# Optimization experiments

Hardware: AMD Instinct MI355X
Metric: run time of the kernel (lower is better)

## Reference

```python
import jax, jax.numpy as jnp
import numpy as np

NQ = 10          # num_qubits
NL = 4           # num_layers (StronglyEntanglingLayers)
DIM = 2 ** NQ    # state-vector dimension = input_linear out features
B = 4096
SEQ = 512
PRED = 96

# ---- static basis-state bookkeeping (wire 0 = most significant bit, as in PennyLane) ----

def _cnot_perm(control, target):
    s = np.arange(DIM)
    bit = (s >> (NQ - 1 - control)) & 1
    return s ^ (bit << (NQ - 1 - target))

def _layer_perms():
    # StronglyEntanglingLayers default ranges: r_l = (l % (n_wires - 1)) + 1,
    # then CNOT(i, (i+r) % n) for i = 0..n-1, applied sequentially.
    perms = []
    for l in range(NL):
        r = (l % (NQ - 1)) + 1
        comp = np.arange(DIM)
        for c in range(NQ):
            g = _cnot_perm(c, (c + r) % NQ)
            comp = comp[g]          # compose: state_new[t] = state_old[comp[t]]
        perms.append(jnp.asarray(comp))
    return perms

PERMS = _layer_perms()

_bits = (np.arange(DIM)[:, None] >> (NQ - 1 - np.arange(NQ))[None, :]) & 1
SIGNS = jnp.asarray(1.0 - 2.0 * _bits, dtype=np.float32)   # [DIM, NQ] PauliZ eigenvalues


def _rot_gates(w):
    # PennyLane Rot(phi, theta, omega) = RZ(omega) @ RY(theta) @ RZ(phi); w: [L, n, 3]
    phi, theta, omega = w[..., 0], w[..., 1], w[..., 2]
    c = jnp.cos(theta / 2)
    s = jnp.sin(theta / 2)
    ep = jnp.exp(0.5j * (phi + omega))   # e^{+i(phi+omega)/2}
    em = jnp.exp(0.5j * (phi - omega))   # e^{+i(phi-omega)/2}
    m00 = jnp.conj(ep) * c
    m01 = -em * s
    m10 = jnp.conj(em) * s
    m11 = ep * c
    return jnp.stack([jnp.stack([m00, m01], -1),
                      jnp.stack([m10, m11], -1)], -2)       # [L, n, 2, 2] complex64


def _apply_1q(psi, U, wire):
    # psi: [B, DIM] complex; apply 2x2 U on `wire`
    b = psi.shape[0]
    left = 2 ** wire
    right = 2 ** (NQ - 1 - wire)
    psi = psi.reshape(b, left, 2, right)
    psi = jnp.einsum('ba,kpaq->kpbq', U, psi)
    return psi.reshape(b, DIM)


def _circuit(psi, q_weights):
    mats = _rot_gates(q_weights)
    for l in range(NL):
        for w in range(NQ):
            psi = _apply_1q(psi, mats[l, w], w)
        psi = psi[:, PERMS[l]]          # composed CNOT ring of this layer
    return psi


def reference(x, W_in, b_in, q_weights, W_out, b_out):
    h = x @ W_in.T + b_in + 1e-6                          # input_linear, then +1e-6
    norm = jnp.linalg.norm(h, axis=-1, keepdims=True)
    psi = (h / norm).astype(jnp.complex64)                # AmplitudeEmbedding(normalize=True)
    psi = _circuit(psi, q_weights)                        # StronglyEntanglingLayers
    probs = psi.real ** 2 + psi.imag ** 2
    expvals = probs @ SIGNS                               # [B, NQ] PauliZ expvals
    return expvals @ W_out.T + b_out                      # output_linear


def setup_inputs() -> dict:
    key = jax.random.key(0)
    ks = jax.random.split(key, 6)
    x = jax.random.normal(ks[0], (B, SEQ), dtype=jnp.float32)
    W_in = jax.random.normal(ks[1], (DIM, SEQ), dtype=jnp.float32) / np.sqrt(SEQ)
    b_in = jax.random.normal(ks[2], (DIM,), dtype=jnp.float32) * 0.01
    q_weights = jax.random.uniform(ks[3], (NL, NQ, 3), dtype=jnp.float32,
                                   minval=0.0, maxval=2.0 * np.pi)
    W_out = jax.random.normal(ks[4], (PRED, NQ), dtype=jnp.float32) / np.sqrt(NQ)
    b_out = jax.random.normal(ks[5], (PRED,), dtype=jnp.float32) * 0.01
    return {"x": x, "W_in": W_in, "b_in": b_in, "q_weights": q_weights,
            "W_out": W_out, "b_out": b_out}
```

## Files before the change

### kernel.cpp

```cpp
#include <hip/hip_runtime.h>
#include <math.h>

#define DIM 1024
#define NQ 10
#define NL 4
#define SEQ 512
#define NROWS 4096
#define PRED 96

typedef unsigned short ushort_t;
typedef unsigned int uint_t;
using half8   = __attribute__((ext_vector_type(8))) _Float16;
using float4v = __attribute__((ext_vector_type(4))) float;

__device__ inline ushort_t f2h(float f) { _Float16 h = (_Float16)f; return *(ushort_t*)&h; }
__device__ inline uint_t pkh(float a, float b) {
    _Float16 ha = (_Float16)a, hb = (_Float16)b;
    return (uint_t)(*(ushort_t*)&ha) | ((uint_t)(*(ushort_t*)&hb) << 16);
}

#define CVT_BLOCKS 1024
#define TRN_BLOCKS 128

__global__ __launch_bounds__(256)
void convert_x_kernel(const float* __restrict__ x, ushort_t* __restrict__ xh,
                      const float* __restrict__ Wi, float* __restrict__ WiT)
{
    __shared__ float t[64][65];
    const int tid = threadIdx.x;
    const int bid = blockIdx.x;

    if (bid < CVT_BLOCKS) {
        int i = (bid * 256 + tid) * 8;
        float4 a = *(const float4*)(x + i);
        float4 b = *(const float4*)(x + i + 4);
        uint4 o;
        o.x = pkh(a.x, a.y); o.y = pkh(a.z, a.w);
        o.z = pkh(b.x, b.y); o.w = pkh(b.z, b.w);
        *(uint4*)(xh + i) = o;
    } else {
        const int b = bid - CVT_BLOCKS;
        const int s0 = (b & 15) * 64;
        const int j0 = (b >> 4) * 64;
        {
            const int r = tid >> 2, cs = (tid & 3) * 16;
            const float* src = Wi + (size_t)(s0 + r) * SEQ + j0 + cs;
            float4 v0 = *(const float4*)(src);
            float4 v1 = *(const float4*)(src + 4);
            float4 v2 = *(const float4*)(src + 8);
            float4 v3 = *(const float4*)(src + 12);
            t[r][cs + 0] = v0.x; t[r][cs + 1] = v0.y; t[r][cs + 2] = v0.z; t[r][cs + 3] = v0.w;
            t[r][cs + 4] = v1.x; t[r][cs + 5] = v1.y; t[r][cs + 6] = v1.z; t[r][cs + 7] = v1.w;
            t[r][cs + 8] = v2.x; t[r][cs + 9] = v2.y; t[r][cs +10] = v2.z; t[r][cs +11] = v2.w;
            t[r][cs +12] = v3.x; t[r][cs +13] = v3.y; t[r][cs +14] = v3.z; t[r][cs +15] = v3.w;
        }
        __syncthreads();
        {
            const int jj = tid >> 2, ss = (tid & 3) * 16;
            float* dst = WiT + (size_t)(j0 + jj) * DIM + s0 + ss;
#pragma unroll
            for (int seg = 0; seg < 4; ++seg) {
                float4 o;
                o.x = t[ss + seg * 4 + 0][jj];
                o.y = t[ss + seg * 4 + 1][jj];
                o.z = t[ss + seg * 4 + 2][jj];
                o.w = t[ss + seg * 4 + 3][jj];
                *(float4*)(dst + seg * 4) = o;
            }
        }
    }
}

__global__ __launch_bounds__(256)
void circuit_hybrid_kernel(const float* __restrict__ WiT, const float* __restrict__ b_in,
                           const float* __restrict__ qw,
                           ushort_t* __restrict__ Crt_r, ushort_t* __restrict__ Crt_i,
                           float* __restrict__ dr, float* __restrict__ di)
{
    __shared__ float gm[NL * NQ][8];
    __shared__ float bre[2][DIM];
    __shared__ float bim[2][DIM];

    const int tid = threadIdx.x;
    const int j = blockIdx.x;

    if (tid < NL * NQ) {
        float phi = qw[tid * 3 + 0], theta = qw[tid * 3 + 1], omega = qw[tid * 3 + 2];
        float ch = cosf(theta * 0.5f), sh = sinf(theta * 0.5f);
        float a = 0.5f * (phi + omega), b = 0.5f * (phi - omega);
        float ca = cosf(a), sa = sinf(a);
        float cb = cosf(b), sb = sinf(b);
        gm[tid][0] =  ch * ca;  gm[tid][1] = -ch * sa;
        gm[tid][2] = -sh * cb;  gm[tid][3] = -sh * sb;
        gm[tid][4] =  sh * cb;  gm[tid][5] = -sh * sb;
        gm[tid][6] =  ch * ca;  gm[tid][7] =  ch * sa;
    }

    float2 st[4];
    if (j < SEQ) {
        float4 wv = *(const float4*)(WiT + (size_t)j * DIM + tid * 4);
        st[0] = make_float2(wv.x, 0.f);
        st[1] = make_float2(wv.y, 0.f);
        st[2] = make_float2(wv.z, 0.f);
        st[3] = make_float2(wv.w, 0.f);
    } else {
#pragma unroll
        for (int r = 0; r < 4; ++r)
            st[r] = make_float2(b_in[tid * 4 + r] + 1e-6f, 0.f);
    }
#pragma unroll
    for (int r = 0; r < 4; ++r) {
        bre[0][r * 256 + tid] = st[r].x;
        bim[0][r * 256 + tid] = st[r].y;
    }
    __syncthreads();
    int cur = 0;

    {
        const float* m = gm[0];
        const int hi = tid >> 7;
        float cAr = hi ? m[6] : m[0], cAi = hi ? m[7] : m[1];
        float cBr = hi ? m[4] : m[2], cBi = hi ? m[5] : m[3];
#pragma unroll
        for (int r = 0; r < 4; ++r) {
            float px = bre[cur][r * 256 + (tid ^ 128)];
            float py = bim[cur][r * 256 + (tid ^ 128)];
            float nx = cAr * st[r].x - cAi * st[r].y + cBr * px - cBi * py;
            float ny = cAr * st[r].y + cAi * st[r].x + cBr * py + cBi * px;
            st[r] = make_float2(nx, ny);
        }
    }

#pragma unroll
    for (int l = 0; l < NL; ++l) {
        {
#pragma unroll
            for (int r = 0; r < 4; ++r) {
                bre[cur ^ 1][r * 256 + tid] = st[r].x;
                bim[cur ^ 1][r * 256 + tid] = st[r].y;
            }
            __syncthreads();
            cur ^= 1;
            const float* m = gm[l * NQ + 1];
            const int hi = (tid >> 6) & 1;
            float cAr = hi ? m[6] : m[0], cAi = hi ? m[7] : m[1];
            float cBr = hi ? m[4] : m[2], cBi = hi ? m[5] : m[3];
#pragma unroll
            for (int r = 0; r < 4; ++r) {
                float px = bre[cur][r * 256 + (tid ^ 64)];
                float py = bim[cur][r * 256 + (tid ^ 64)];
                float nx = cAr * st[r].x - cAi * st[r].y + cBr * px - cBi * py;
                float ny = cAr * st[r].y + cAi * st[r].x + cBr * py + cBi * px;
                st[r] = make_float2(nx, ny);
            }
        }
#pragma unroll
        for (int w = 2; w < 8; ++w) {
            const float* m = gm[l * NQ + w];
            const int lb = 7 - w;
            const int hi = (tid >> lb) & 1;
            float cAr = hi ? m[6] : m[0], cAi = hi ? m[7] : m[1];
            float cBr = hi ? m[4] : m[2], cBi = hi ? m[5] : m[3];
            const int mask = 1 << lb;
#pragma unroll
            for (int r = 0; r < 4; ++r) {
                float px = __shfl_xor(st[r].x, mask, 64);
                float py = __shfl_xor(st[r].y, mask, 64);
                float nx = cAr * st[r].x - cAi * st[r].y + cBr * px - cBi * py;
                float ny = cAr * st[r].y + cAi * st[r].x + cBr * py + cBi * px;
                st[r] = make_float2(nx, ny);
            }
        }
        {
            const float* m = gm[l * NQ + 8];
            float m00r = m[0], m00i = m[1], m01r = m[2], m01i = m[3];
            float m10r = m[4], m10i = m[5], m11r = m[6], m11i = m[7];
#pragma unroll
            for (int r0 = 0; r0 < 2; ++r0) {
                float2 a0 = st[r0], a1 = st[r0 + 2];
                st[r0].x     = m00r * a0.x - m00i * a0.y + m01r * a1.x - m01i * a1.y;
                st[r0].y     = m00r * a0.y + m00i * a0.x + m01r * a1.y + m01i * a1.x;
                st[r0 + 2].x = m10r * a0.x - m10i * a0.y + m11r * a1.x - m11i * a1.y;
                st[r0 + 2].y = m10r * a0.y + m10i * a0.x + m11r * a1.y + m11i * a1.x;
            }
        }
        {
            const float* m = gm[l * NQ + 9];
            float m00r = m[0], m00i = m[1], m01r = m[2], m01i = m[3];
            float m10r = m[4], m10i = m[5], m11r = m[6], m11i = m[7];
#pragma unroll
            for (int r0 = 0; r0 < 4; r0 += 2) {
                float2 a0 = st[r0], a1 = st[r0 + 1];
                st[r0].x     = m00r * a0.x - m00i * a0.y + m01r * a1.x - m01i * a1.y;
                st[r0].y     = m00r * a0.y + m00i * a0.x + m01r * a1.y + m01i * a1.x;
                st[r0 + 1].x = m10r * a0.x - m10i * a0.y + m11r * a1.x - m11i * a1.y;
                st[r0 + 1].y = m10r * a0.y + m10i * a0.x + m11r * a1.y + m11i * a1.x;
            }
        }
        {
#pragma unroll
            for (int r = 0; r < 4; ++r) {
                bre[cur ^ 1][r * 256 + tid] = st[r].x;
                bim[cur ^ 1][r * 256 + tid] = st[r].y;
            }
            __syncthreads();
            cur ^= 1;

            const int rr = l % (NQ - 1) + 1;
            int pbase = tid * 4;
            int p1 = 1, p2 = 2, p512 = 512;
#pragma unroll
            for (int c = 9; c >= 0; --c) {
                const int t = (c + rr) % NQ;
                pbase ^= ((pbase >> (9 - c)) & 1) << (9 - t);
                p1    ^= ((p1    >> (9 - c)) & 1) << (9 - t);
                p2    ^= ((p2    >> (9 - c)) & 1) << (9 - t);
                p512  ^= ((p512  >> (9 - c)) & 1) << (9 - t);
            }
            const int p3 = p1 ^ p2;
            int Ps[4] = {pbase, pbase ^ p1, pbase ^ p2, pbase ^ p3};

            if (l < NL - 1) {
                const float* m = gm[(l + 1) * NQ + 0];
                const int hi = tid >> 7;
                float cAr = hi ? m[6] : m[0], cAi = hi ? m[7] : m[1];
                float cBr = hi ? m[4] : m[2], cBi = hi ? m[5] : m[3];
#pragma unroll
                for (int r = 0; r < 4; ++r) {
                    int so = Ps[r];
                    int sp = so ^ p512;
                    int io = (so >> 2) | ((so & 3) << 8);
                    int ip = (sp >> 2) | ((sp & 3) << 8);
                    float ox = bre[cur][io], oy = bim[cur][io];
                    float px = bre[cur][ip], py = bim[cur][ip];
                    float nx = cAr * ox - cAi * oy + cBr * px - cBi * py;
                    float ny = cAr * oy + cAi * ox + cBr * py + cBi * px;
                    st[r] = make_float2(nx, ny);
                }
            } else {
#pragma unroll
                for (int r = 0; r < 4; ++r) {
                    int so = Ps[r];
                    int io = (so >> 2) | ((so & 3) << 8);
                    st[r] = make_float2(bre[cur][io], bim[cur][io]);
                }
            }
        }
    }

    if (j < SEQ) {
#pragma unroll
        for (int r = 0; r < 4; ++r) {
            Crt_r[(size_t)(tid * 4 + r) * SEQ + j] = f2h(st[r].x);
            Crt_i[(size_t)(tid * 4 + r) * SEQ + j] = f2h(st[r].y);
        }
    } else {
#pragma unroll
        for (int r = 0; r < 4; ++r) {
            dr[tid * 4 + r] = st[r].x;
            di[tid * 4 + r] = st[r].y;
        }
    }
}

#define GBM 128
#define GBNC 64
#define GBK 64
#define LDA 72
#define LDP 65

__global__ __launch_bounds__(256)
void gemm_fused_kernel(const ushort_t* __restrict__ xh,
                       const ushort_t* __restrict__ Crt_r, const ushort_t* __restrict__ Crt_i,
                       const float* __restrict__ dr, const float* __restrict__ di,
                       float* __restrict__ part)
{
    __shared__ __align__(16) char lds[(GBM + 2 * GBNC) * LDA * 2];
    ushort_t* Ash = (ushort_t*)lds;
    ushort_t* Bsr = Ash + GBM * LDA;
    ushort_t* Bsi = Bsr + GBNC * LDA;
    float*    Ps  = (float*)lds;
    __shared__ float drs[GBNC], dis[GBNC];

    const int tid = threadIdx.x;
    const int bm = blockIdx.x, bn = blockIdx.y;
    const int lane = tid & 63, wv = tid >> 6;
    const int n0 = bn * GBNC;

    if (tid < GBNC) { drs[tid] = dr[n0 + tid]; dis[tid] = di[n0 + tid]; }

    float4v accr[2][4], acci[2][4];
#pragma unroll
    for (int a = 0; a < 2; ++a)
#pragma unroll
        for (int b = 0; b < 4; ++b) { accr[a][b] = (float4v)0.f; acci[a][b] = (float4v)0.f; }

    const int sr = tid >> 1, ko = (tid & 1) * 32;
    const ushort_t* xa = xh + (size_t)(bm * GBM + sr) * SEQ + ko;
    const int bsel = tid >> 7;
    const int nr = (tid & 127) >> 1;
    const int bko = (tid & 1) * 32;
    const ushort_t* bsrc = (bsel ? Crt_i : Crt_r) + (size_t)(n0 + nr) * SEQ + bko;
    ushort_t* bdst = (bsel ? Bsi : Bsr) + nr * LDA + bko;

    const int fm = lane & 15, kq = (lane >> 4) * 8;
    const int wrow = wv * 32;

    for (int k0 = 0; k0 < SEQ; k0 += GBK) {
        uint4 a0 = *(const uint4*)(xa + k0);
        uint4 a1 = *(const uint4*)(xa + k0 + 8);
        uint4 a2 = *(const uint4*)(xa + k0 + 16);
        uint4 a3 = *(const uint4*)(xa + k0 + 24);
        *(uint4*)(Ash + sr * LDA + ko)      = a0;
        *(uint4*)(Ash + sr * LDA + ko + 8)  = a1;
        *(uint4*)(Ash + sr * LDA + ko + 16) = a2;
        *(uint4*)(Ash + sr * LDA + ko + 24) = a3;
        uint4 b0 = *(const uint4*)(bsrc + k0);
        uint4 b1 = *(const uint4*)(bsrc + k0 + 8);
        uint4 b2 = *(const uint4*)(bsrc + k0 + 16);
        uint4 b3 = *(const uint4*)(bsrc + k0 + 24);
        *(uint4*)bdst        = b0;
        *(uint4*)(bdst + 8)  = b1;
        *(uint4*)(bdst + 16) = b2;
        *(uint4*)(bdst + 24) = b3;
        __syncthreads();

        {
            half8 ah0 = *(half8*)(Ash + (wrow + fm) * LDA + kq);
            half8 ah1 = *(half8*)(Ash + (wrow + 16 + fm) * LDA + kq);
#pragma unroll
            for (int nt = 0; nt < 4; ++nt) {
                half8 br = *(half8*)(Bsr + (nt * 16 + fm) * LDA + kq);
                half8 bi = *(half8*)(Bsi + (nt * 16 + fm) * LDA + kq);
                accr[0][nt] = __builtin_amdgcn_mfma_f32_16x16x32_f16(ah0, br, accr[0][nt], 0, 0, 0);
                accr[1][nt] = __builtin_amdgcn_mfma_f32_16x16x32_f16(ah1, br, accr[1][nt], 0, 0, 0);
                acci[0][nt] = __builtin_amdgcn_mfma_f32_16x16x32_f16(ah0, bi, acci[0][nt], 0, 0, 0);
                acci[1][nt] = __builtin_amdgcn_mfma_f32_16x16x32_f16(ah1, bi, acci[1][nt], 0, 0, 0);
            }
        }
        {
            half8 ah0 = *(half8*)(Ash + (wrow + fm) * LDA + 32 + kq);
            half8 ah1 = *(half8*)(Ash + (wrow + 16 + fm) * LDA + 32 + kq);
#pragma unroll
            for (int nt = 0; nt < 4; ++nt) {
                half8 br = *(half8*)(Bsr + (nt * 16 + fm) * LDA + 32 + kq);
                half8 bi = *(half8*)(Bsi + (nt * 16 + fm) * LDA + 32 + kq);
                accr[0][nt] = __builtin_amdgcn_mfma_f32_16x16x32_f16(ah0, br, accr[0][nt], 0, 0, 0);
                accr[1][nt] = __builtin_amdgcn_mfma_f32_16x16x32_f16(ah1, br, accr[1][nt], 0, 0, 0);
                acci[0][nt] = __builtin_amdgcn_mfma_f32_16x16x32_f16(ah0, bi, acci[0][nt], 0, 0, 0);
                acci[1][nt] = __builtin_amdgcn_mfma_f32_16x16x32_f16(ah1, bi, acci[1][nt], 0, 0, 0);
            }
        }
        __syncthreads();
    }

    const int rq = (lane >> 4) * 4;
#pragma unroll
    for (int mt = 0; mt < 2; ++mt)
#pragma unroll
        for (int nt = 0; nt < 4; ++nt) {
            float drv = drs[nt * 16 + fm], div = dis[nt * 16 + fm];
#pragma unroll
            for (int reg = 0; reg < 4; ++reg) {
                int lrow = wrow + mt * 16 + rq + reg;
                float zr = accr[mt][nt][reg] + drv;
                float zi = acci[mt][nt][reg] + div;
                Ps[lrow * LDP + nt * 16 + fm] = zr * zr + zi * zi;
            }
        }
    __syncthreads();

    {
        const int row = tid >> 1, hh = tid & 1;
        const float* pr = Ps + row * LDP + hh * 32;
        float nrm = 0.f, e0 = 0.f, e1 = 0.f, e2 = 0.f, e3 = 0.f, e4 = 0.f, e5 = 0.f;
#pragma unroll
        for (int i = 0; i < 32; ++i) {
            float p = pr[i];
            int c = hh * 32 + i;
            nrm += p;
            e0 += ((c >> 5) & 1) ? -p : p;
            e1 += ((c >> 4) & 1) ? -p : p;
            e2 += ((c >> 3) & 1) ? -p : p;
            e3 += ((c >> 2) & 1) ? -p : p;
            e4 += ((c >> 1) & 1) ? -p : p;
            e5 += (c & 1) ? -p : p;
        }
        size_t base2 = ((size_t)(bm * GBM + row) * 32 + (bn * 2 + hh)) * 8;
        part[base2 + 0] = nrm;
        part[base2 + 1] = e0; part[base2 + 2] = e1; part[base2 + 3] = e2;
        part[base2 + 4] = e3; part[base2 + 5] = e4; part[base2 + 6] = e5;
    }
}

__global__ __launch_bounds__(256)
void finalize_kernel(const float* __restrict__ part, const float* __restrict__ W_out,
                     const float* __restrict__ b_out, float* __restrict__ out)
{
    __shared__ float evf[4][10];
    const int tid = threadIdx.x;
    const int lane = tid & 63, wv = tid >> 6;
    const int row0 = blockIdx.x * 4;
    const int row = row0 + wv;

    {
        float v[11];
        if (lane < 32) {
            const float* p = part + ((size_t)row * 32 + lane) * 8;
            float4 a = *(const float4*)p;
            float4 b = *(const float4*)(p + 4);
            float nrm = a.x;
            int bnn = lane >> 1;
            v[0] = nrm;
            v[1] = (bnn & 8) ? -nrm : nrm;
            v[2] = (bnn & 4) ? -nrm : nrm;
            v[3] = (bnn & 2) ? -nrm : nrm;
            v[4] = (bnn & 1) ? -nrm : nrm;
            v[5] = a.y; v[6] = a.z; v[7] = a.w;
            v[8] = b.x; v[9] = b.y; v[10] = b.z;
        } else {
#pragma unroll
            for (int k = 0; k < 11; ++k) v[k] = 0.f;
        }
#pragma unroll
        for (int m = 16; m; m >>= 1)
#pragma unroll
            for (int k = 0; k < 11; ++k) v[k] += __shfl_xor(v[k], m, 64);
        if (lane == 0) {
            float inv = 1.0f / v[0];
#pragma unroll
            for (int k = 0; k < 10; ++k) evf[wv][k] = v[k + 1] * inv;
        }
    }
    __syncthreads();

    for (int it = tid; it < 4 * PRED; it += 256) {
        int rr = it / PRED, cc = it - rr * PRED;
        float o = b_out[cc];
#pragma unroll
        for (int k = 0; k < NQ; ++k) o = fmaf(W_out[cc * NQ + k], evf[rr][k], o);
        out[(size_t)(row0 + rr) * PRED + cc] = o;
    }
}

extern "C" void kernel_launch(void* const* d_in, const int* in_sizes, int n_in,
                              void* d_out, int out_size, void* d_ws, size_t ws_size,
                              hipStream_t stream) {
    const float* x     = (const float*)d_in[0];
    const float* W_in  = (const float*)d_in[1];
    const float* b_in  = (const float*)d_in[2];
    const float* qw    = (const float*)d_in[3];
    const float* W_out = (const float*)d_in[4];
    const float* b_out = (const float*)d_in[5];
    float* out = (float*)d_out;

    char* w = (char*)d_ws;
    const size_t MB = 1u << 20;
    ushort_t* xh    = (ushort_t*)w;
    ushort_t* Crt_r = (ushort_t*)(w + 4 * MB);
    ushort_t* Crt_i = (ushort_t*)(w + 5 * MB);
    float*    dr    = (float*)(w + 6 * MB);
    float*    di    = dr + DIM;
    float*    part  = (float*)(w + 7 * MB);
    float*    WiT   = (float*)(w + 11 * MB);

    convert_x_kernel<<<CVT_BLOCKS + TRN_BLOCKS, 256, 0, stream>>>(x, xh, W_in, WiT);
    circuit_hybrid_kernel<<<SEQ + 1, 256, 0, stream>>>(WiT, b_in, qw, Crt_r, Crt_i, dr, di);
    dim3 g2(NROWS / GBM, DIM / GBNC);
    gemm_fused_kernel<<<g2, 256, 0, stream>>>(xh, Crt_r, Crt_i, dr, di, part);
    finalize_kernel<<<NROWS / 4, 256, 0, stream>>>(part, W_out, b_out, out);
}
```

Measured before the change: 108.8 us.

## Fuse fp32-to-fp16 conversion of x into GEMM load and halve K tile

The separate pass that converted x to fp16 in a workspace buffer is removed. The GEMM now reads fp32 x directly and packs it to fp16 while staging into LDS, and the K tile shrinks from 64 to 32 so the staging stays within budget. This saves one full write and re-read of the fp16 copy of x. In exchange, each of the 16 column-blocks re-reads x at fp32 width, which doubles A-side global traffic, and the loop runs twice as many iterations and barriers.

```diff
diff --git a/kernel.cpp b/kernel.cpp
--- a/kernel.cpp
+++ b/kernel.cpp
@@ -19,54 +19,40 @@
     return (uint_t)(*(ushort_t*)&ha) | ((uint_t)(*(ushort_t*)&hb) << 16);
 }
 
-#define CVT_BLOCKS 1024
 #define TRN_BLOCKS 128
 
 __global__ __launch_bounds__(256)
-void convert_x_kernel(const float* __restrict__ x, ushort_t* __restrict__ xh,
-                      const float* __restrict__ Wi, float* __restrict__ WiT)
+void transpose_w_kernel(const float* __restrict__ Wi, float* __restrict__ WiT)
 {
     __shared__ float t[64][65];
     const int tid = threadIdx.x;
-    const int bid = blockIdx.x;
-
-    if (bid < CVT_BLOCKS) {
-        int i = (bid * 256 + tid) * 8;
-        float4 a = *(const float4*)(x + i);
-        float4 b = *(const float4*)(x + i + 4);
-        uint4 o;
-        o.x = pkh(a.x, a.y); o.y = pkh(a.z, a.w);
-        o.z = pkh(b.x, b.y); o.w = pkh(b.z, b.w);
-        *(uint4*)(xh + i) = o;
-    } else {
-        const int b = bid - CVT_BLOCKS;
-        const int s0 = (b & 15) * 64;
-        const int j0 = (b >> 4) * 64;
-        {
-            const int r = tid >> 2, cs = (tid & 3) * 16;
-            const float* src = Wi + (size_t)(s0 + r) * SEQ + j0 + cs;
-            float4 v0 = *(const float4*)(src);
-            float4 v1 = *(const float4*)(src + 4);
-            float4 v2 = *(const float4*)(src + 8);
-            float4 v3 = *(const float4*)(src + 12);
-            t[r][cs + 0] = v0.x; t[r][cs + 1] = v0.y; t[r][cs + 2] = v0.z; t[r][cs + 3] = v0.w;
-            t[r][cs + 4] = v1.x; t[r][cs + 5] = v1.y; t[r][cs + 6] = v1.z; t[r][cs + 7] = v1.w;
-            t[r][cs + 8] = v2.x; t[r][cs + 9] = v2.y; t[r][cs +10] = v2.z; t[r][cs +11] = v2.w;
-            t[r][cs +12] = v3.x; t[r][cs +13] = v3.y; t[r][cs +14] = v3.z; t[r][cs +15] = v3.w;
-        }
-        __syncthreads();
-        {
-            const int jj = tid >> 2, ss = (tid & 3) * 16;
-            float* dst = WiT + (size_t)(j0 + jj) * DIM + s0 + ss;
-#pragma unroll
-            for (int seg = 0; seg < 4; ++seg) {
-                float4 o;
-                o.x = t[ss + seg * 4 + 0][jj];
-                o.y = t[ss + seg * 4 + 1][jj];
-                o.z = t[ss + seg * 4 + 2][jj];
-                o.w = t[ss + seg * 4 + 3][jj];
-                *(float4*)(dst + seg * 4) = o;
-            }
+    const int b = blockIdx.x;
+    const int s0 = (b & 15) * 64;
+    const int j0 = (b >> 4) * 64;
+    {
+        const int r = tid >> 2, cs = (tid & 3) * 16;
+        const float* src = Wi + (size_t)(s0 + r) * SEQ + j0 + cs;
+        float4 v0 = *(const float4*)(src);
+        float4 v1 = *(const float4*)(src + 4);
+        float4 v2 = *(const float4*)(src + 8);
+        float4 v3 = *(const float4*)(src + 12);
+        t[r][cs + 0] = v0.x; t[r][cs + 1] = v0.y; t[r][cs + 2] = v0.z; t[r][cs + 3] = v0.w;
+        t[r][cs + 4] = v1.x; t[r][cs + 5] = v1.y; t[r][cs + 6] = v1.z; t[r][cs + 7] = v1.w;
+        t[r][cs + 8] = v2.x; t[r][cs + 9] = v2.y; t[r][cs +10] = v2.z; t[r][cs +11] = v2.w;
+        t[r][cs +12] = v3.x; t[r][cs +13] = v3.y; t[r][cs +14] = v3.z; t[r][cs +15] = v3.w;
+    }
+    __syncthreads();
+    {
+        const int jj = tid >> 2, ss = (tid & 3) * 16;
+        float* dst = WiT + (size_t)(j0 + jj) * DIM + s0 + ss;
+#pragma unroll
+        for (int seg = 0; seg < 4; ++seg) {
+            float4 o;
+            o.x = t[ss + seg * 4 + 0][jj];
+            o.y = t[ss + seg * 4 + 1][jj];
+            o.z = t[ss + seg * 4 + 2][jj];
+            o.w = t[ss + seg * 4 + 3][jj];
+            *(float4*)(dst + seg * 4) = o;
         }
     }
 }
@@ -265,17 +251,17 @@
 
 #define GBM 128
 #define GBNC 64
-#define GBK 64
-#define LDA 72
+#define GBK 32
+#define LDA 40
 #define LDP 65
 
 __global__ __launch_bounds__(256)
-void gemm_fused_kernel(const ushort_t* __restrict__ xh,
+void gemm_fused_kernel(const float* __restrict__ x,
                        const ushort_t* __restrict__ Crt_r, const ushort_t* __restrict__ Crt_i,
                        const float* __restrict__ dr, const float* __restrict__ di,
                        float* __restrict__ part)
 {
-    __shared__ __align__(16) char lds[(GBM + 2 * GBNC) * LDA * 2];
+    __shared__ __align__(16) char lds[GBM * LDP * 4];
     ushort_t* Ash = (ushort_t*)lds;
     ushort_t* Bsr = Ash + GBM * LDA;
     ushort_t* Bsi = Bsr + GBNC * LDA;
@@ -295,11 +281,11 @@
 #pragma unroll
         for (int b = 0; b < 4; ++b) { accr[a][b] = (float4v)0.f; acci[a][b] = (float4v)0.f; }
 
-    const int sr = tid >> 1, ko = (tid & 1) * 32;
-    const ushort_t* xa = xh + (size_t)(bm * GBM + sr) * SEQ + ko;
+    const int sr = tid >> 1, ko = (tid & 1) * 16;
+    const float* xa = x + (size_t)(bm * GBM + sr) * SEQ + ko;
     const int bsel = tid >> 7;
     const int nr = (tid & 127) >> 1;
-    const int bko = (tid & 1) * 32;
+    const int bko = (tid & 1) * 16;
     const ushort_t* bsrc = (bsel ? Crt_i : Crt_r) + (size_t)(n0 + nr) * SEQ + bko;
     ushort_t* bdst = (bsel ? Bsi : Bsr) + nr * LDA + bko;
 
@@ -307,49 +293,33 @@
     const int wrow = wv * 32;
 
     for (int k0 = 0; k0 < SEQ; k0 += GBK) {
-        uint4 a0 = *(const uint4*)(xa + k0);
-        uint4 a1 = *(const uint4*)(xa + k0 + 8);
-        uint4 a2 = *(const uint4*)(xa + k0 + 16);
-        uint4 a3 = *(const uint4*)(xa + k0 + 24);
-        *(uint4*)(Ash + sr * LDA + ko)      = a0;
-        *(uint4*)(Ash + sr * LDA + ko + 8)  = a1;
-        *(uint4*)(Ash + sr * LDA + ko + 16) = a2;
-        *(uint4*)(Ash + sr * LDA + ko + 24) = a3;
+        float4 f0 = *(const float4*)(xa + k0);
+        float4 f1 = *(const float4*)(xa + k0 + 4);
+        float4 f2 = *(const float4*)(xa + k0 + 8);
+        float4 f3 = *(const float4*)(xa + k0 + 12);
+        uint4 a0, a1;
+        a0.x = pkh(f0.x, f0.y); a0.y = pkh(f0.z, f0.w);
+        a0.z = pkh(f1.x, f1.y); a0.w = pkh(f1.z, f1.w);
+        a1.x = pkh(f2.x, f2.y); a1.y = pkh(f2.z, f2.w);
+        a1.z = pkh(f3.x, f3.y); a1.w = pkh(f3.z, f3.w);
+        *(uint4*)(Ash + sr * LDA + ko)     = a0;
+        *(uint4*)(Ash + sr * LDA + ko + 8) = a1;
         uint4 b0 = *(const uint4*)(bsrc + k0);
         uint4 b1 = *(const uint4*)(bsrc + k0 + 8);
-        uint4 b2 = *(const uint4*)(bsrc + k0 + 16);
-        uint4 b3 = *(const uint4*)(bsrc + k0 + 24);
-        *(uint4*)bdst        = b0;
-        *(uint4*)(bdst + 8)  = b1;
-        *(uint4*)(bdst + 16) = b2;
-        *(uint4*)(bdst + 24) = b3;
+        *(uint4*)bdst       = b0;
+        *(uint4*)(bdst + 8) = b1;
         __syncthreads();
 
-        {
-            half8 ah0 = *(half8*)(Ash + (wrow + fm) * LDA + kq);
-            half8 ah1 = *(half8*)(Ash + (wrow + 16 + fm) * LDA + kq);
-#pragma unroll
-            for (int nt = 0; nt < 4; ++nt) {
-                half8 br = *(half8*)(Bsr + (nt * 16 + fm) * LDA + kq);
-                half8 bi = *(half8*)(Bsi + (nt * 16 + fm) * LDA + kq);
-                accr[0][nt] = __builtin_amdgcn_mfma_f32_16x16x32_f16(ah0, br, accr[0][nt], 0, 0, 0);
-                accr[1][nt] = __builtin_amdgcn_mfma_f32_16x16x32_f16(ah1, br, accr[1][nt], 0, 0, 0);
-                acci[0][nt] = __builtin_amdgcn_mfma_f32_16x16x32_f16(ah0, bi, acci[0][nt], 0, 0, 0);
-                acci[1][nt] = __builtin_amdgcn_mfma_f32_16x16x32_f16(ah1, bi, acci[1][nt], 0, 0, 0);
-            }
-        }
-        {
-            half8 ah0 = *(half8*)(Ash + (wrow + fm) * LDA + 32 + kq);
-            half8 ah1 = *(half8*)(Ash + (wrow + 16 + fm) * LDA + 32 + kq);
-#pragma unroll
-            for (int nt = 0; nt < 4; ++nt) {
-                half8 br = *(half8*)(Bsr + (nt * 16 + fm) * LDA + 32 + kq);
-                half8 bi = *(half8*)(Bsi + (nt * 16 + fm) * LDA + 32 + kq);
-                accr[0][nt] = __builtin_amdgcn_mfma_f32_16x16x32_f16(ah0, br, accr[0][nt], 0, 0, 0);
-                accr[1][nt] = __builtin_amdgcn_mfma_f32_16x16x32_f16(ah1, br, accr[1][nt], 0, 0, 0);
-                acci[0][nt] = __builtin_amdgcn_mfma_f32_16x16x32_f16(ah0, bi, acci[0][nt], 0, 0, 0);
-                acci[1][nt] = __builtin_amdgcn_mfma_f32_16x16x32_f16(ah1, bi, acci[1][nt], 0, 0, 0);
-            }
+        half8 ah0 = *(half8*)(Ash + (wrow + fm) * LDA + kq);
+        half8 ah1 = *(half8*)(Ash + (wrow + 16 + fm) * LDA + kq);
+#pragma unroll
+        for (int nt = 0; nt < 4; ++nt) {
+            half8 br = *(half8*)(Bsr + (nt * 16 + fm) * LDA + kq);
+            half8 bi = *(half8*)(Bsi + (nt * 16 + fm) * LDA + kq);
+            accr[0][nt] = __builtin_amdgcn_mfma_f32_16x16x32_f16(ah0, br, accr[0][nt], 0, 0, 0);
+            accr[1][nt] = __builtin_amdgcn_mfma_f32_16x16x32_f16(ah1, br, accr[1][nt], 0, 0, 0);
+            acci[0][nt] = __builtin_amdgcn_mfma_f32_16x16x32_f16(ah0, bi, acci[0][nt], 0, 0, 0);
+            acci[1][nt] = __builtin_amdgcn_mfma_f32_16x16x32_f16(ah1, bi, acci[1][nt], 0, 0, 0);
         }
         __syncthreads();
     }
@@ -456,17 +426,16 @@
 
     char* w = (char*)d_ws;
     const size_t MB = 1u << 20;
-    ushort_t* xh    = (ushort_t*)w;
-    ushort_t* Crt_r = (ushort_t*)(w + 4 * MB);
-    ushort_t* Crt_i = (ushort_t*)(w + 5 * MB);
-    float*    dr    = (float*)(w + 6 * MB);
+    ushort_t* Crt_r = (ushort_t*)w;
+    ushort_t* Crt_i = (ushort_t*)(w + 1 * MB);
+    float*    dr    = (float*)(w + 2 * MB);
     float*    di    = dr + DIM;
-    float*    part  = (float*)(w + 7 * MB);
-    float*    WiT   = (float*)(w + 11 * MB);
-
-    convert_x_kernel<<<CVT_BLOCKS + TRN_BLOCKS, 256, 0, stream>>>(x, xh, W_in, WiT);
+    float*    part  = (float*)(w + 3 * MB);
+    float*    WiT   = (float*)(w + 7 * MB);
+
+    transpose_w_kernel<<<TRN_BLOCKS, 256, 0, stream>>>(W_in, WiT);
     circuit_hybrid_kernel<<<SEQ + 1, 256, 0, stream>>>(WiT, b_in, qw, Crt_r, Crt_i, dr, di);
     dim3 g2(NROWS / GBM, DIM / GBNC);
-    gemm_fused_kernel<<<g2, 256, 0, stream>>>(xh, Crt_r, Crt_i, dr, di, part);
+    gemm_fused_kernel<<<g2, 256, 0, stream>>>(x, Crt_r, Crt_i, dr, di, part);
     finalize_kernel<<<NROWS / 4, 256, 0, stream>>>(part, W_out, b_out, out);
 }
```

After: 110.7 us. Within noise of the previous version (+1.7%).
